# Optimization experiments

Hardware: AMD Instinct MI355X
Metric: run time of the kernel (lower is better)

## Reference

```python
import jax, jax.numpy as jnp
import numpy as np

B, S, D = 2, 2048, 2048
H, KV, HD = 32, 8, 64          # n_heads, n_kv_heads, head_dim
REP = H // KV                  # 4
THETA = 10000.0


def _rotate_half(u):
    h = u.shape[-1] // 2
    return jnp.concatenate([-u[..., h:], u[..., :h]], axis=-1)


def setup_inputs() -> dict:
    key = jax.random.key(0)
    ks = jax.random.split(key, 5)
    x = jax.random.normal(ks[0], (B, S, D), dtype=jnp.float32)
    Wq = jax.random.normal(ks[1], (D, H * HD), dtype=jnp.float32) * 0.02
    Wk = jax.random.normal(ks[2], (D, KV * HD), dtype=jnp.float32) * 0.02
    Wv = jax.random.normal(ks[3], (D, KV * HD), dtype=jnp.float32) * 0.02
    Wo = jax.random.normal(ks[4], (H * HD, D), dtype=jnp.float32) * 0.02
    return {"x": x, "Wq": Wq, "Wk": Wk, "Wv": Wv, "Wo": Wo}


def reference(x, Wq, Wk, Wv, Wo):
    b, s, d = x.shape
    # QKV projections (nn.Linear, no bias)
    q = (x @ Wq).reshape(b, s, H, HD).transpose(0, 2, 1, 3)   # [B,H,S,HD]
    k = (x @ Wk).reshape(b, s, KV, HD).transpose(0, 2, 1, 3)  # [B,KV,S,HD]
    v = (x @ Wv).reshape(b, s, KV, HD).transpose(0, 2, 1, 3)  # [B,KV,S,HD]

    # RoPE (position_offset = 0)
    inv_freq = 1.0 / (THETA ** (jnp.arange(0, HD, 2, dtype=jnp.float32) / HD))
    freqs = jnp.outer(jnp.arange(s, dtype=jnp.float32), inv_freq)  # [S,HD/2]
    emb = jnp.concatenate([freqs, freqs], axis=-1)                  # [S,HD]
    cos, sin = jnp.cos(emb), jnp.sin(emb)
    q = q * cos + _rotate_half(q) * sin
    k = k * cos + _rotate_half(k) * sin

    # Grouped attention: avoid materializing repeated KV tensors.
    qg = q.reshape(b, KV, REP, s, HD)                               # [B,KV,REP,S,HD]
    scale = 1.0 / np.sqrt(HD)
    scores = jnp.einsum('bgrqd,bgkd->bgrqk', qg, k) * scale         # [B,KV,REP,S,S]
    causal = jnp.tril(jnp.ones((s, s), dtype=bool))
    scores = jnp.where(causal, scores, jnp.finfo(jnp.float32).min)
    probs = jax.nn.softmax(scores.astype(jnp.float32), axis=-1).astype(q.dtype)
    out = jnp.einsum('bgrqk,bgkd->bgrqd', probs, v)                 # [B,KV,REP,S,HD]
    out = out.reshape(b, H, s, HD).transpose(0, 2, 1, 3).reshape(b, s, H * HD)
    return out @ Wo                                                  # [B,S,D]
```

## Files before the change

### kernel.cpp

```cpp
#include <hip/hip_runtime.h>
#include <math.h>

typedef __bf16 bf16_t;
typedef bf16_t bf16x8 __attribute__((ext_vector_type(8)));
typedef bf16_t bf16x4 __attribute__((ext_vector_type(4)));
typedef float floatx4 __attribute__((ext_vector_type(4)));
typedef short short4v __attribute__((ext_vector_type(4)));

#define MFMA16(a, b, c) __builtin_amdgcn_mfma_f32_16x16x32_bf16((a), (b), (c), 0, 0, 0)

#if __has_builtin(__builtin_amdgcn_exp2f)
#define PEXP(x) __builtin_amdgcn_exp2f(x)
#define SCORE_SCALE (0.125f * 1.4426950408889634f)
#else
#define PEXP(x) __expf(x)
#define SCORE_SCALE 0.125f
#endif

#if __has_builtin(__builtin_amdgcn_mfma_f32_16x16x16bf16_1k)
#define HAVE_MFMA_K16 1
__device__ __forceinline__ floatx4 mfma_k16(bf16x4 a, bf16x4 b, floatx4 c)
{
    union { bf16x4 v; short4v s; } ua, ub;
    ua.v = a; ub.v = b;
    return __builtin_amdgcn_mfma_f32_16x16x16bf16_1k(ua.s, ub.s, c, 0, 0, 0);
}
#endif

union PU { unsigned u[2]; bf16x4 v; };
union BU { unsigned u[4]; bf16x8 v; };

__device__ __forceinline__ void gld16(const void* g, void* lds)
{
    __builtin_amdgcn_global_load_lds(
        reinterpret_cast<const __attribute__((address_space(1))) void*>(
            reinterpret_cast<uintptr_t>(g)),
        reinterpret_cast<__attribute__((address_space(3))) void*>(
            (unsigned int)reinterpret_cast<uintptr_t>(lds)),
        16, 0, 0);
}

template <int ROUNDS>
__device__ __forceinline__ void stage512(
    const bf16_t* __restrict__ g, int K, int row0, int k0,
    bf16_t* lds, int tid, int wave)
{
    #pragma unroll
    for (int i = 0; i < ROUNDS; ++i) {
        int c = i * 512 + tid;
        int r = c >> 3, s = c & 7;
        gld16(g + (size_t)(row0 + r) * K + k0 + ((s ^ (r & 7)) << 3),
              lds + (size_t)(i * 512 + wave * 64) * 8);
    }
}

template <typename TC, int BN>
__device__ __forceinline__ void gemm256_body(
    const bf16_t* __restrict__ A, const bf16_t* __restrict__ Bt,
    TC* __restrict__ C, int row0, int col0, int N, int K, bf16_t* smem)
{
    constexpr int NT = BN / 64;
    constexpr int RB = BN / 64;
    constexpr int LPT = 4 + RB;

    const int tid  = threadIdx.x;
    const int wave = tid >> 6, lane = tid & 63;
    const int quad = lane >> 4, l16 = lane & 15;
    const int wm = (wave >> 2) * 128;
    const int wn = (wave & 3) * (BN / 4);

    bf16_t* As0 = smem;
    bf16_t* As1 = smem + 256 * 64;
    bf16_t* Bs0 = smem + 2 * 256 * 64;
    bf16_t* Bs1 = Bs0 + BN * 64;

    floatx4 acc[8][NT] = {};

    const int ntile = K >> 6;

    stage512<4>(A, K, row0, 0, As0, tid, wave);
    stage512<RB>(Bt, K, col0, 0, Bs0, tid, wave);

    #pragma unroll 1
    for (int t = 0; t < ntile; ++t) {
        const int cur = t & 1;
        bf16_t* Asc = cur ? As1 : As0;
        bf16_t* Bsc = cur ? Bs1 : Bs0;
        bf16_t* Asn = cur ? As0 : As1;
        bf16_t* Bsn = cur ? Bs0 : Bs1;

        if (t + 1 < ntile) {
            stage512<4>(A, K, row0, (t + 1) << 6, Asn, tid, wave);
            stage512<RB>(Bt, K, col0, (t + 1) << 6, Bsn, tid, wave);
            if constexpr (LPT == 8)
                __asm__ volatile("s_waitcnt vmcnt(8)" ::: "memory");
            else
                __asm__ volatile("s_waitcnt vmcnt(6)" ::: "memory");
        } else {
            __asm__ volatile("s_waitcnt vmcnt(0)" ::: "memory");
        }
        __builtin_amdgcn_s_barrier();
        __asm__ volatile("" ::: "memory");

        #pragma unroll
        for (int kh = 0; kh < 2; ++kh) {
            bf16x8 af[8], bfr[NT];
            #pragma unroll
            for (int mt = 0; mt < 8; ++mt) {
                int ar = wm + mt * 16 + l16;
                af[mt] = *(const bf16x8*)&Asc[ar * 64 + (((kh * 4 + quad) ^ (ar & 7)) << 3)];
            }
            #pragma unroll
            for (int nt = 0; nt < NT; ++nt) {
                int br = wn + nt * 16 + l16;
                bfr[nt] = *(const bf16x8*)&Bsc[br * 64 + (((kh * 4 + quad) ^ (br & 7)) << 3)];
            }
            __builtin_amdgcn_s_setprio(1);
            #pragma unroll
            for (int mt = 0; mt < 8; ++mt)
                #pragma unroll
                for (int nt = 0; nt < NT; ++nt)
                    acc[mt][nt] = MFMA16(af[mt], bfr[nt], acc[mt][nt]);
            __builtin_amdgcn_s_setprio(0);
        }
        __asm__ volatile("s_waitcnt lgkmcnt(0)" ::: "memory");
        __builtin_amdgcn_s_barrier();
    }

    #pragma unroll
    for (int mt = 0; mt < 8; ++mt)
        #pragma unroll
        for (int nt = 0; nt < NT; ++nt)
            #pragma unroll
            for (int r = 0; r < 4; ++r)
                C[(size_t)(row0 + wm + mt * 16 + quad * 4 + r) * N
                  + col0 + wn + nt * 16 + l16] = (TC)acc[mt][nt][r];
}

__global__ __launch_bounds__(512, 2) void gemm256_qkv(
    const bf16_t* __restrict__ A, const bf16_t* __restrict__ BtQ,
    const bf16_t* __restrict__ BtK, const bf16_t* __restrict__ BtV,
    bf16_t* __restrict__ CQ, bf16_t* __restrict__ CK, bf16_t* __restrict__ CV)
{
    extern __shared__ __align__(16) bf16_t smem[];
    const int x = blockIdx.x;
    const bf16_t* Bt; bf16_t* C; int N, col0;
    if (x < 8)       { Bt = BtQ; C = CQ; N = 2048; col0 = x * 256; }
    else if (x < 10) { Bt = BtK; C = CK; N = 512;  col0 = (x - 8) * 256; }
    else             { Bt = BtV; C = CV; N = 512;  col0 = (x - 10) * 256; }
    gemm256_body<bf16_t, 256>(A, Bt, C, blockIdx.y * 256, col0, N, 2048, smem);
}

__global__ __launch_bounds__(512, 2) void gemm256_out(
    const bf16_t* __restrict__ A, const bf16_t* __restrict__ Bt,
    float* __restrict__ C)
{
    extern __shared__ __align__(16) bf16_t smem[];
    gemm256_body<float, 128>(A, Bt, C, blockIdx.y * 256, blockIdx.x * 128,
                             2048, 2048, smem);
}

__device__ __forceinline__ void transpose_body(
    const float* __restrict__ W, bf16_t* __restrict__ Wt, int K, int N,
    int bx, int by, float (*t)[33], int tid)
{
    int tx = tid & 31, ty = tid >> 5;
    #pragma unroll
    for (int i = 0; i < 32; i += 8)
        t[ty + i][tx] = W[(size_t)(by + ty + i) * N + bx + tx];
    __syncthreads();
    #pragma unroll
    for (int i = 0; i < 32; i += 8)
        Wt[(size_t)(bx + ty + i) * K + by + tx] = (bf16_t)t[tx][ty + i];
}

__global__ __launch_bounds__(256) void prep_all(
    const float* __restrict__ x, const float* __restrict__ Wq,
    const float* __restrict__ Wk, const float* __restrict__ Wv,
    bf16_t* __restrict__ xb, bf16_t* __restrict__ WqT,
    bf16_t* __restrict__ WkT, bf16_t* __restrict__ WvT)
{
    __shared__ float t[32][33];
    const int blk = blockIdx.x, tid = threadIdx.x;
    if (blk < 8192) {
        int i = blk * 256 + tid;
        float4 f = ((const float4*)x)[i];
        bf16x4 v = {(bf16_t)f.x, (bf16_t)f.y, (bf16_t)f.z, (bf16_t)f.w};
        ((bf16x4*)xb)[i] = v;
    } else if (blk < 12288) {
        int r = blk - 8192;
        transpose_body(Wq, WqT, 2048, 2048, (r & 63) * 32, (r >> 6) * 32, t, tid);
    } else if (blk < 13312) {
        int r = blk - 12288;
        transpose_body(Wk, WkT, 2048, 512, (r & 15) * 32, (r >> 4) * 32, t, tid);
    } else {
        int r = blk - 13312;
        transpose_body(Wv, WvT, 2048, 512, (r & 15) * 32, (r >> 4) * 32, t, tid);
    }
}

__global__ __launch_bounds__(256) void mid_all(
    bf16_t* __restrict__ Kw, const bf16_t* __restrict__ Vw,
    bf16_t* __restrict__ VtG, const float* __restrict__ Wo,
    bf16_t* __restrict__ WoT)
{
    __shared__ float tf[32][33];
    __shared__ bf16_t tb[32][34];
    const int blk = blockIdx.x, tid = threadIdx.x;
    if (blk < 4096) {
        int idx = blk * 256 + tid;
        int i   = idx & 31;
        int h   = (idx >> 5) & 7;
        int row = idx >> 8;
        int pos = row & 2047;
        float invf = powf(10000.0f, -(float)i / 32.0f);
        float sv, cv;
        sincosf((float)pos * invf, &sv, &cv);
        size_t base = (size_t)row * 512 + (size_t)h * 64 + i;
        float a  = (float)Kw[base];
        float b2 = (float)Kw[base + 32];
        Kw[base]      = (bf16_t)(a * cv - b2 * sv);
        Kw[base + 32] = (bf16_t)(b2 * cv + a * sv);
    } else if (blk < 6144) {
        int r  = blk - 4096;
        int bz = r >> 10, r2 = r & 1023;
        int bx = (r2 & 15) * 32, by = (r2 >> 4) * 32;
        int tx = tid & 31, ty = tid >> 5;
        #pragma unroll
        for (int i = 0; i < 32; i += 8)
            tb[ty + i][tx] = Vw[((size_t)bz * 2048 + by + ty + i) * 512 + bx + tx];
        __syncthreads();
        #pragma unroll
        for (int i = 0; i < 32; i += 8)
            VtG[((size_t)bz * 512 + bx + ty + i) * 2048 + by + tx] = tb[tx][ty + i];
    } else {
        int r = blk - 6144;
        transpose_body(Wo, WoT, 2048, 2048, (r & 63) * 32, (r >> 6) * 32, tf, tid);
    }
}

__global__ __launch_bounds__(256) void gqa_attn(
    const bf16_t* __restrict__ Q, const bf16_t* __restrict__ Kc,
    const bf16_t* __restrict__ Vt, bf16_t* __restrict__ AO)
{
    __shared__ alignas(16) bf16_t Ks[2][64 * 64];
    __shared__ alignas(16) bf16_t Vs[2][64 * 64];

    const int x = blockIdx.x, h = blockIdx.y, b = blockIdx.z, g = h >> 2;
    const int tid  = threadIdx.x;
    const int wave = tid >> 6, lane = tid & 63;
    const int quad = lane >> 4, l16 = lane & 15;

    #pragma unroll 1
    for (int t = 0; t < 2; ++t) {
        const int qt = t ? x : (15 - x);
        const int q0 = qt * 128;
        int qb[2];
        qb[0] = q0 + wave * 16;
        qb[1] = qb[0] + 64;

        bf16x8 qf[2][2];
        #pragma unroll
        for (int mt = 0; mt < 2; ++mt) {
            int qrow = qb[mt] + l16;
            const bf16_t* qp = Q + (size_t)(b * 2048 + qrow) * 2048 + h * 64 + quad * 8;
            bf16x8 lo = *(const bf16x8*)qp;
            bf16x8 hi = *(const bf16x8*)(qp + 32);
            #pragma unroll
            for (int j = 0; j < 8; ++j) {
                int d = quad * 8 + j;
                float invf = powf(10000.0f, -(float)d / 32.0f);
                float sv, cv;
                sincosf((float)qrow * invf, &sv, &cv);
                float a = (float)lo[j], c2 = (float)hi[j];
                qf[mt][0][j] = (bf16_t)((a * cv - c2 * sv) * SCORE_SCALE);
                qf[mt][1][j] = (bf16_t)((c2 * cv + a * sv) * SCORE_SCALE);
            }
        }

        floatx4 o[2][4] = {};
        floatx4 ls4[2] = {};

        const int ktmax = 2 * qt + 1;

        __asm__ volatile("s_waitcnt lgkmcnt(0)" ::: "memory");
        __builtin_amdgcn_s_barrier();
        #pragma unroll
        for (int i = 0; i < 2; ++i) {
            int c = i * 256 + tid;
            int r = c >> 3, s = c & 7;
            int sw = (s ^ (r & 7)) << 3;
            gld16(Kc + (size_t)(b * 2048 + r) * 512 + g * 64 + sw,
                  &Ks[0][(i * 256 + wave * 64) * 8]);
            gld16(Vt + (size_t)(b * 512 + g * 64 + r) * 2048 + sw,
                  &Vs[0][(i * 256 + wave * 64) * 8]);
        }

        #pragma unroll 1
        for (int kt = 0; kt <= ktmax; ++kt) {
            const int cur = kt & 1;
            if (kt < ktmax) {
                const int kn = kt + 1;
                #pragma unroll
                for (int i = 0; i < 2; ++i) {
                    int c = i * 256 + tid;
                    int r = c >> 3, s = c & 7;
                    int sw = (s ^ (r & 7)) << 3;
                    gld16(Kc + (size_t)(b * 2048 + kn * 64 + r) * 512 + g * 64 + sw,
                          &Ks[cur ^ 1][(i * 256 + wave * 64) * 8]);
                    gld16(Vt + (size_t)(b * 512 + g * 64 + r) * 2048 + kn * 64 + sw,
                          &Vs[cur ^ 1][(i * 256 + wave * 64) * 8]);
                }
                __asm__ volatile("s_waitcnt vmcnt(4)" ::: "memory");
            } else {
                __asm__ volatile("s_waitcnt vmcnt(0)" ::: "memory");
            }
            __builtin_amdgcn_s_barrier();

            bool en[2];
            en[0] = (kt * 64) <= (qb[0] + 15);
            en[1] = (kt * 64) <= (qb[1] + 15);

            floatx4 st[2][4] = {};
            #pragma unroll
            for (int nt = 0; nt < 4; ++nt) {
                int kr = nt * 16 + l16;
                bf16x8 kf0 = *(const bf16x8*)&Ks[cur][kr * 64 + ((quad ^ (kr & 7)) << 3)];
                bf16x8 kf1 = *(const bf16x8*)&Ks[cur][kr * 64 + (((4 + quad) ^ (kr & 7)) << 3)];
                if (en[0]) {
                    st[0][nt] = MFMA16(kf0, qf[0][0], st[0][nt]);
                    st[0][nt] = MFMA16(kf1, qf[0][1], st[0][nt]);
                }
                if (en[1]) {
                    st[1][nt] = MFMA16(kf0, qf[1][0], st[1][nt]);
                    st[1][nt] = MFMA16(kf1, qf[1][1], st[1][nt]);
                }
            }

            PU pk[2][4];
            #pragma unroll
            for (int mt = 0; mt < 2; ++mt) {
                if (!en[mt]) continue;
                const bool diag = (kt * 64 + 63) > qb[mt];
                const int qa = qb[mt] + l16;
                #pragma unroll
                for (int nt = 0; nt < 4; ++nt) {
                    float pv[4];
                    #pragma unroll
                    for (int r = 0; r < 4; ++r) {
                        float e = PEXP(st[mt][nt][r]);
                        if (diag) {
                            int ka = kt * 64 + nt * 16 + quad * 4 + r;
                            if (ka > qa) e = 0.f;
                        }
                        ls4[mt][r] += e;
                        pv[r] = e;
                    }
                    pk[mt][nt].v = bf16x4{(bf16_t)pv[0], (bf16_t)pv[1],
                                          (bf16_t)pv[2], (bf16_t)pv[3]};
                }
            }

#ifdef HAVE_MFMA_K16
            #pragma unroll
            for (int nt = 0; nt < 4; ++nt)
                #pragma unroll
                for (int dt = 0; dt < 4; ++dt) {
                    int vr = dt * 16 + l16;
                    int slot = ((nt << 1) | (quad >> 1)) ^ (vr & 7);
                    bf16x4 va = *(const bf16x4*)&Vs[cur][vr * 64 + (slot << 3)
                                                         + ((quad & 1) << 2)];
                    if (en[0]) o[0][dt] = mfma_k16(va, pk[0][nt].v, o[0][dt]);
                    if (en[1]) o[1][dt] = mfma_k16(va, pk[1][nt].v, o[1][dt]);
                }
#else
            #pragma unroll
            for (int H = 0; H < 2; ++H) {
                BU bfv[2];
                #pragma unroll
                for (int mt = 0; mt < 2; ++mt) {
                    if (!en[mt]) continue;
                    #pragma unroll
                    for (int j = 0; j < 4; ++j) {
                        int srcl = (((quad & 1) << 1) + (j >> 1)) * 16 + l16;
                        unsigned a0 = (unsigned)__shfl((int)pk[mt][2 * H].u[j & 1], srcl, 64);
                        unsigned a1 = (unsigned)__shfl((int)pk[mt][2 * H + 1].u[j & 1], srcl, 64);
                        bfv[mt].u[j] = (quad >> 1) ? a1 : a0;
                    }
                }
                #pragma unroll
                for (int dt = 0; dt < 4; ++dt) {
                    int vr = dt * 16 + l16;
                    bf16x8 va = *(const bf16x8*)&Vs[cur][vr * 64
                                  + ((((H << 2) | quad) ^ (vr & 7)) << 3)];
                    if (en[0]) o[0][dt] = MFMA16(va, bfv[0].v, o[0][dt]);
                    if (en[1]) o[1][dt] = MFMA16(va, bfv[1].v, o[1][dt]);
                }
            }
#endif
            __asm__ volatile("s_waitcnt lgkmcnt(0)" ::: "memory");
            __builtin_amdgcn_s_barrier();
        }

        #pragma unroll
        for (int mt = 0; mt < 2; ++mt) {
            float l = ls4[mt][0] + ls4[mt][1] + ls4[mt][2] + ls4[mt][3];
            l += __shfl_xor(l, 16, 64);
            l += __shfl_xor(l, 32, 64);
            float rc = 1.0f / l;
            #pragma unroll
            for (int dt = 0; dt < 4; ++dt) {
                bf16x4 ov = {(bf16_t)(o[mt][dt][0] * rc), (bf16_t)(o[mt][dt][1] * rc),
                             (bf16_t)(o[mt][dt][2] * rc), (bf16_t)(o[mt][dt][3] * rc)};
                *(bf16x4*)&AO[(size_t)(b * 2048 + qb[mt] + l16) * 2048
                              + h * 64 + dt * 16 + quad * 4] = ov;
            }
        }
    }
}

extern "C" void kernel_launch(void* const* d_in, const int* in_sizes, int n_in,
                              void* d_out, int out_size, void* d_ws, size_t ws_size,
                              hipStream_t stream)
{
    const float* x  = (const float*)d_in[0];
    const float* Wq = (const float*)d_in[1];
    const float* Wk = (const float*)d_in[2];
    const float* Wv = (const float*)d_in[3];
    const float* Wo = (const float*)d_in[4];
    float* out = (float*)d_out;

    const size_t MB = 1024 * 1024;
    char* ws = (char*)d_ws;
    bf16_t* xb_AO = (bf16_t*)(ws);
    bf16_t* WqoT  = (bf16_t*)(ws + 16 * MB);
    bf16_t* WkT   = (bf16_t*)(ws + 24 * MB);
    bf16_t* WvT   = (bf16_t*)(ws + 26 * MB);
    bf16_t* Qw    = (bf16_t*)(ws + 28 * MB);
    bf16_t* Kw    = (bf16_t*)(ws + 44 * MB);
    bf16_t* Vw    = (bf16_t*)(ws + 48 * MB);
    bf16_t* VtG   = (bf16_t*)(ws + 52 * MB);

    static bool s_attr = false;
    if (!s_attr) {
        hipFuncSetAttribute(reinterpret_cast<const void*>(gemm256_qkv),
                            hipFuncAttributeMaxDynamicSharedMemorySize, 131072);
        hipFuncSetAttribute(reinterpret_cast<const void*>(gemm256_out),
                            hipFuncAttributeMaxDynamicSharedMemorySize, 98304);
        s_attr = true;
    }

    prep_all<<<14336, 256, 0, stream>>>(x, Wq, Wk, Wv, xb_AO, WqoT, WkT, WvT);

    gemm256_qkv<<<dim3(12, 16), 512, 131072, stream>>>(
        xb_AO, WqoT, WkT, WvT, Qw, Kw, Vw);

    mid_all<<<10240, 256, 0, stream>>>(Kw, Vw, VtG, Wo, WqoT);

    gqa_attn<<<dim3(8, 32, 2), 256, 0, stream>>>(Qw, Kw, VtG, xb_AO);

    gemm256_out<<<dim3(16, 16), 512, 98304, stream>>>(xb_AO, WqoT, out);
}
```

Before: 312.7 us.

## Split GEMM tile load schedule across half-steps and shrink attention query tiles

The GEMM main loop now splits each k-tile into two N-halves. The B tile for the next step and the A tile two steps ahead are issued at different barriers, so global-to-LDS loads overlap with the MFMA work in a finer-grained way. The attention kernel drops from 128-row query tiles (two 64-row halves with enable masks) to 64-row tiles, doubling the grid to 16x32x2 blocks. This removes the per-half causal predicates and improves load balance and occupancy, but each K/V tile is now reloaded for twice as many query blocks.

```diff
diff --git a/kernel.cpp b/kernel.cpp
--- a/kernel.cpp
+++ b/kernel.cpp
@@ -40,16 +40,15 @@
         16, 0, 0);
 }
 
-template <int ROUNDS>
-__device__ __forceinline__ void stage512(
-    const bf16_t* __restrict__ g, int K, int row0, int k0,
+template <int RND>
+__device__ __forceinline__ void stageT(
+    const bf16_t* __restrict__ g, int K, int r0, int k0,
     bf16_t* lds, int tid, int wave)
 {
     #pragma unroll
-    for (int i = 0; i < ROUNDS; ++i) {
-        int c = i * 512 + tid;
-        int r = c >> 3, s = c & 7;
-        gld16(g + (size_t)(row0 + r) * K + k0 + ((s ^ (r & 7)) << 3),
+    for (int i = 0; i < RND; ++i) {
+        int c = i * 512 + tid, r = c >> 3, s = c & 7;
+        gld16(g + (size_t)(r0 + r) * K + k0 + ((s ^ (r & 7)) << 3),
               lds + (size_t)(i * 512 + wave * 64) * 8);
     }
 }
@@ -60,8 +59,8 @@
     TC* __restrict__ C, int row0, int col0, int N, int K, bf16_t* smem)
 {
     constexpr int NT = BN / 64;
+    constexpr int NH = NT / 2;
     constexpr int RB = BN / 64;
-    constexpr int LPT = 4 + RB;
 
     const int tid  = threadIdx.x;
     const int wave = tid >> 6, lane = tid & 63;
@@ -74,57 +73,85 @@
     bf16_t* Bs0 = smem + 2 * 256 * 64;
     bf16_t* Bs1 = Bs0 + BN * 64;
 
+    const int ntile = K >> 6;
+
     floatx4 acc[8][NT] = {};
 
-    const int ntile = K >> 6;
-
-    stage512<4>(A, K, row0, 0, As0, tid, wave);
-    stage512<RB>(Bt, K, col0, 0, Bs0, tid, wave);
+    stageT<4>(A, K, row0, 0, As0, tid, wave);
+    stageT<RB>(Bt, K, col0, 0, Bs0, tid, wave);
+    stageT<4>(A, K, row0, 64, As1, tid, wave);
 
     #pragma unroll 1
-    for (int t = 0; t < ntile; ++t) {
-        const int cur = t & 1;
-        bf16_t* Asc = cur ? As1 : As0;
-        bf16_t* Bsc = cur ? Bs1 : Bs0;
-        bf16_t* Asn = cur ? As0 : As1;
-        bf16_t* Bsn = cur ? Bs0 : Bs1;
-
-        if (t + 1 < ntile) {
-            stage512<4>(A, K, row0, (t + 1) << 6, Asn, tid, wave);
-            stage512<RB>(Bt, K, col0, (t + 1) << 6, Bsn, tid, wave);
-            if constexpr (LPT == 8)
-                __asm__ volatile("s_waitcnt vmcnt(8)" ::: "memory");
-            else
-                __asm__ volatile("s_waitcnt vmcnt(6)" ::: "memory");
-        } else {
+    for (int u = 0; u < ntile; ++u) {
+        const int d = u & 1;
+        bf16_t* Asd = d ? As1 : As0;
+        bf16_t* Bsd = d ? Bs1 : Bs0;
+
+        if (u + 1 < ntile)
+            __asm__ volatile("s_waitcnt vmcnt(4)" ::: "memory");
+        else
             __asm__ volatile("s_waitcnt vmcnt(0)" ::: "memory");
-        }
         __builtin_amdgcn_s_barrier();
         __asm__ volatile("" ::: "memory");
 
-        #pragma unroll
-        for (int kh = 0; kh < 2; ++kh) {
-            bf16x8 af[8], bfr[NT];
-            #pragma unroll
-            for (int mt = 0; mt < 8; ++mt) {
+        if (u + 1 < ntile)
+            stageT<RB>(Bt, K, col0, (u + 1) << 6, d ? Bs0 : Bs1, tid, wave);
+
+        bf16x8 af[8][2], bfr[NH][2];
+        #pragma unroll
+        for (int mt = 0; mt < 8; ++mt)
+            #pragma unroll
+            for (int kh = 0; kh < 2; ++kh) {
                 int ar = wm + mt * 16 + l16;
-                af[mt] = *(const bf16x8*)&Asc[ar * 64 + (((kh * 4 + quad) ^ (ar & 7)) << 3)];
-            }
-            #pragma unroll
-            for (int nt = 0; nt < NT; ++nt) {
-                int br = wn + nt * 16 + l16;
-                bfr[nt] = *(const bf16x8*)&Bsc[br * 64 + (((kh * 4 + quad) ^ (br & 7)) << 3)];
-            }
-            __builtin_amdgcn_s_setprio(1);
+                af[mt][kh] = *(const bf16x8*)&Asd[ar * 64 +
+                    (((kh * 4 + quad) ^ (ar & 7)) << 3)];
+            }
+        #pragma unroll
+        for (int j = 0; j < NH; ++j)
+            #pragma unroll
+            for (int kh = 0; kh < 2; ++kh) {
+                int br = wn + j * 16 + l16;
+                bfr[j][kh] = *(const bf16x8*)&Bsd[br * 64 +
+                    (((kh * 4 + quad) ^ (br & 7)) << 3)];
+            }
+
+        __builtin_amdgcn_s_setprio(1);
+        #pragma unroll
+        for (int kh = 0; kh < 2; ++kh)
             #pragma unroll
             for (int mt = 0; mt < 8; ++mt)
                 #pragma unroll
-                for (int nt = 0; nt < NT; ++nt)
-                    acc[mt][nt] = MFMA16(af[mt], bfr[nt], acc[mt][nt]);
-            __builtin_amdgcn_s_setprio(0);
-        }
+                for (int j = 0; j < NH; ++j)
+                    acc[mt][j] = MFMA16(af[mt][kh], bfr[j][kh], acc[mt][j]);
+        __builtin_amdgcn_s_setprio(0);
+
         __asm__ volatile("s_waitcnt lgkmcnt(0)" ::: "memory");
         __builtin_amdgcn_s_barrier();
+        __asm__ volatile("" ::: "memory");
+
+        if (u + 2 < ntile)
+            stageT<4>(A, K, row0, (u + 2) << 6, Asd, tid, wave);
+
+        bf16x8 bf1[NH][2];
+        #pragma unroll
+        for (int j = 0; j < NH; ++j)
+            #pragma unroll
+            for (int kh = 0; kh < 2; ++kh) {
+                int br = wn + (NH + j) * 16 + l16;
+                bf1[j][kh] = *(const bf16x8*)&Bsd[br * 64 +
+                    (((kh * 4 + quad) ^ (br & 7)) << 3)];
+            }
+
+        __builtin_amdgcn_s_setprio(1);
+        #pragma unroll
+        for (int kh = 0; kh < 2; ++kh)
+            #pragma unroll
+            for (int mt = 0; mt < 8; ++mt)
+                #pragma unroll
+                for (int j = 0; j < NH; ++j)
+                    acc[mt][NH + j] = MFMA16(af[mt][kh], bf1[j][kh],
+                                             acc[mt][NH + j]);
+        __builtin_amdgcn_s_setprio(0);
     }
 
     #pragma unroll
@@ -253,16 +280,12 @@
 
     #pragma unroll 1
     for (int t = 0; t < 2; ++t) {
-        const int qt = t ? x : (15 - x);
-        const int q0 = qt * 128;
-        int qb[2];
-        qb[0] = q0 + wave * 16;
-        qb[1] = qb[0] + 64;
-
-        bf16x8 qf[2][2];
-        #pragma unroll
-        for (int mt = 0; mt < 2; ++mt) {
-            int qrow = qb[mt] + l16;
+        const int qt = t ? x : (31 - x);
+        const int qb = qt * 64 + wave * 16;
+
+        bf16x8 qf[2];
+        {
+            int qrow = qb + l16;
             const bf16_t* qp = Q + (size_t)(b * 2048 + qrow) * 2048 + h * 64 + quad * 8;
             bf16x8 lo = *(const bf16x8*)qp;
             bf16x8 hi = *(const bf16x8*)(qp + 32);
@@ -273,15 +296,15 @@
                 float sv, cv;
                 sincosf((float)qrow * invf, &sv, &cv);
                 float a = (float)lo[j], c2 = (float)hi[j];
-                qf[mt][0][j] = (bf16_t)((a * cv - c2 * sv) * SCORE_SCALE);
-                qf[mt][1][j] = (bf16_t)((c2 * cv + a * sv) * SCORE_SCALE);
+                qf[0][j] = (bf16_t)((a * cv - c2 * sv) * SCORE_SCALE);
+                qf[1][j] = (bf16_t)((c2 * cv + a * sv) * SCORE_SCALE);
             }
         }
 
-        floatx4 o[2][4] = {};
-        floatx4 ls4[2] = {};
-
-        const int ktmax = 2 * qt + 1;
+        floatx4 o[4] = {};
+        floatx4 ls4 = {};
+
+        const int ktmax = qt;
 
         __asm__ volatile("s_waitcnt lgkmcnt(0)" ::: "memory");
         __builtin_amdgcn_s_barrier();
@@ -317,47 +340,35 @@
             }
             __builtin_amdgcn_s_barrier();
 
-            bool en[2];
-            en[0] = (kt * 64) <= (qb[0] + 15);
-            en[1] = (kt * 64) <= (qb[1] + 15);
-
-            floatx4 st[2][4] = {};
+            floatx4 st[4] = {};
             #pragma unroll
             for (int nt = 0; nt < 4; ++nt) {
                 int kr = nt * 16 + l16;
                 bf16x8 kf0 = *(const bf16x8*)&Ks[cur][kr * 64 + ((quad ^ (kr & 7)) << 3)];
                 bf16x8 kf1 = *(const bf16x8*)&Ks[cur][kr * 64 + (((4 + quad) ^ (kr & 7)) << 3)];
-                if (en[0]) {
-                    st[0][nt] = MFMA16(kf0, qf[0][0], st[0][nt]);
-                    st[0][nt] = MFMA16(kf1, qf[0][1], st[0][nt]);
-                }
-                if (en[1]) {
-                    st[1][nt] = MFMA16(kf0, qf[1][0], st[1][nt]);
-                    st[1][nt] = MFMA16(kf1, qf[1][1], st[1][nt]);
-                }
-            }
-
-            PU pk[2][4];
-            #pragma unroll
-            for (int mt = 0; mt < 2; ++mt) {
-                if (!en[mt]) continue;
-                const bool diag = (kt * 64 + 63) > qb[mt];
-                const int qa = qb[mt] + l16;
+                st[nt] = MFMA16(kf0, qf[0], st[nt]);
+                st[nt] = MFMA16(kf1, qf[1], st[nt]);
+            }
+
+            PU pk[4];
+            {
+                const bool diag = (kt == qt);
+                const int qa = qb + l16;
                 #pragma unroll
                 for (int nt = 0; nt < 4; ++nt) {
                     float pv[4];
                     #pragma unroll
                     for (int r = 0; r < 4; ++r) {
-                        float e = PEXP(st[mt][nt][r]);
+                        float e = PEXP(st[nt][r]);
                         if (diag) {
                             int ka = kt * 64 + nt * 16 + quad * 4 + r;
                             if (ka > qa) e = 0.f;
                         }
-                        ls4[mt][r] += e;
+                        ls4[r] += e;
                         pv[r] = e;
                     }
-                    pk[mt][nt].v = bf16x4{(bf16_t)pv[0], (bf16_t)pv[1],
-                                          (bf16_t)pv[2], (bf16_t)pv[3]};
+                    pk[nt].v = bf16x4{(bf16_t)pv[0], (bf16_t)pv[1],
+                                      (bf16_t)pv[2], (bf16_t)pv[3]};
                 }
             }
 
@@ -370,31 +381,25 @@
                     int slot = ((nt << 1) | (quad >> 1)) ^ (vr & 7);
                     bf16x4 va = *(const bf16x4*)&Vs[cur][vr * 64 + (slot << 3)
                                                          + ((quad & 1) << 2)];
-                    if (en[0]) o[0][dt] = mfma_k16(va, pk[0][nt].v, o[0][dt]);
-                    if (en[1]) o[1][dt] = mfma_k16(va, pk[1][nt].v, o[1][dt]);
+                    o[dt] = mfma_k16(va, pk[nt].v, o[dt]);
                 }
 #else
             #pragma unroll
             for (int H = 0; H < 2; ++H) {
-                BU bfv[2];
-                #pragma unroll
-                for (int mt = 0; mt < 2; ++mt) {
-                    if (!en[mt]) continue;
-                    #pragma unroll
-                    for (int j = 0; j < 4; ++j) {
-                        int srcl = (((quad & 1) << 1) + (j >> 1)) * 16 + l16;
-                        unsigned a0 = (unsigned)__shfl((int)pk[mt][2 * H].u[j & 1], srcl, 64);
-                        unsigned a1 = (unsigned)__shfl((int)pk[mt][2 * H + 1].u[j & 1], srcl, 64);
-                        bfv[mt].u[j] = (quad >> 1) ? a1 : a0;
-                    }
+                BU bfv;
+                #pragma unroll
+                for (int j = 0; j < 4; ++j) {
+                    int srcl = (((quad & 1) << 1) + (j >> 1)) * 16 + l16;
+                    unsigned a0 = (unsigned)__shfl((int)pk[2 * H].u[j & 1], srcl, 64);
+                    unsigned a1 = (unsigned)__shfl((int)pk[2 * H + 1].u[j & 1], srcl, 64);
+                    bfv.u[j] = (quad >> 1) ? a1 : a0;
                 }
                 #pragma unroll
                 for (int dt = 0; dt < 4; ++dt) {
                     int vr = dt * 16 + l16;
                     bf16x8 va = *(const bf16x8*)&Vs[cur][vr * 64
                                   + ((((H << 2) | quad) ^ (vr & 7)) << 3)];
-                    if (en[0]) o[0][dt] = MFMA16(va, bfv[0].v, o[0][dt]);
-                    if (en[1]) o[1][dt] = MFMA16(va, bfv[1].v, o[1][dt]);
+                    o[dt] = MFMA16(va, bfv.v, o[dt]);
                 }
             }
 #endif
@@ -402,19 +407,16 @@
             __builtin_amdgcn_s_barrier();
         }
 
-        #pragma unroll
-        for (int mt = 0; mt < 2; ++mt) {
-            float l = ls4[mt][0] + ls4[mt][1] + ls4[mt][2] + ls4[mt][3];
-            l += __shfl_xor(l, 16, 64);
-            l += __shfl_xor(l, 32, 64);
-            float rc = 1.0f / l;
-            #pragma unroll
-            for (int dt = 0; dt < 4; ++dt) {
-                bf16x4 ov = {(bf16_t)(o[mt][dt][0] * rc), (bf16_t)(o[mt][dt][1] * rc),
-                             (bf16_t)(o[mt][dt][2] * rc), (bf16_t)(o[mt][dt][3] * rc)};
-                *(bf16x4*)&AO[(size_t)(b * 2048 + qb[mt] + l16) * 2048
-                              + h * 64 + dt * 16 + quad * 4] = ov;
-            }
+        float l = ls4[0] + ls4[1] + ls4[2] + ls4[3];
+        l += __shfl_xor(l, 16, 64);
+        l += __shfl_xor(l, 32, 64);
+        float rc = 1.0f / l;
+        #pragma unroll
+        for (int dt = 0; dt < 4; ++dt) {
+            bf16x4 ov = {(bf16_t)(o[dt][0] * rc), (bf16_t)(o[dt][1] * rc),
+                         (bf16_t)(o[dt][2] * rc), (bf16_t)(o[dt][3] * rc)};
+            *(bf16x4*)&AO[(size_t)(b * 2048 + qb + l16) * 2048
+                          + h * 64 + dt * 16 + quad * 4] = ov;
         }
     }
 }
@@ -457,7 +459,7 @@
 
     mid_all<<<10240, 256, 0, stream>>>(Kw, Vw, VtG, Wo, WqoT);
 
-    gqa_attn<<<dim3(8, 32, 2), 256, 0, stream>>>(Qw, Kw, VtG, xb_AO);
+    gqa_attn<<<dim3(16, 32, 2), 256, 0, stream>>>(Qw, Kw, VtG, xb_AO);
 
     gemm256_out<<<dim3(16, 16), 512, 98304, stream>>>(xb_AO, WqoT, out);
 }
```

Result: faster. 306.1 us (-2.1%).
